# Optimization experiments

Measured on AMD Instinct MI355X. Metric: run time of the kernel, lower is better.

Reference implementation:

```python
import jax, jax.numpy as jnp
import numpy as np

D_IN, D_OUT, K = 128, 128, 64
X_MIN, X_MAX = 0.0, 1.0
EPS = 1e-12


def _pchip_slopes(y, x):
    # y: [..., K], x: [K] strictly increasing -> slopes [..., K]. Assumes K >= 3.
    h = x[1:] - x[:-1]                      # [K-1]
    delta = (y[..., 1:] - y[..., :-1]) / (h + EPS)
    h0, h1 = h[:-1], h[1:]
    w1 = 2.0 * h1 + h0
    w2 = h1 + 2.0 * h0
    d0_, d1_ = delta[..., :-1], delta[..., 1:]
    same_sign = d0_ * d1_ > 0
    denom = w1 / (d0_ + EPS) + w2 / (d1_ + EPS)
    d_int = jnp.where(same_sign, (w1 + w2) / (denom + EPS), 0.0)  # [..., K-2]
    d_first = ((2.0 * h[0] + h[1]) * delta[..., 0] - h[0] * delta[..., 1]) / (h[0] + h[1] + EPS)
    d_last = ((2.0 * h[-1] + h[-2]) * delta[..., -1] - h[-1] * delta[..., -2]) / (h[-1] + h[-2] + EPS)

    def limit(di, de):
        di = jnp.where(di * de <= 0, 0.0, di)
        return jnp.where(jnp.abs(di) > 3.0 * jnp.abs(de), 3.0 * de, di)

    d_first = limit(d_first, delta[..., 0])
    d_last = limit(d_last, delta[..., -1])
    return jnp.concatenate([d_first[..., None], d_int, d_last[..., None]], axis=-1)


def setup_inputs() -> dict:
    key = jax.random.key(0)
    k1, k2 = jax.random.split(key)
    x = jax.random.normal(k1, (4096, D_IN), dtype=jnp.float32)
    coeffs = 0.2 * jax.random.normal(k2, (D_OUT, D_IN, K), dtype=jnp.float32)
    bias = jnp.zeros((D_OUT,), dtype=jnp.float32)
    knots = jnp.linspace(X_MIN, X_MAX, K, dtype=jnp.float32)
    return {"x": x, "coeffs": coeffs, "bias": bias, "knots": knots}


def reference(x, coeffs, bias, knots):
    B = x.shape[0]
    slopes = _pchip_slopes(coeffs, knots)              # [d_out, d_in, K]
    h = (X_MAX - X_MIN) / (K - 1)

    xc = jnp.clip(x, X_MIN, X_MAX)                     # [B, d_in]
    idx = jnp.clip(jnp.floor((xc - X_MIN) / h).astype(jnp.int32), 0, K - 2)
    t = (xc - (X_MIN + idx.astype(x.dtype) * h)) / h   # [B, d_in]
    t2 = t * t
    t3 = t2 * t
    h00 = 2 * t3 - 3 * t2 + 1
    h10 = t3 - 2 * t2 + t
    h01 = -2 * t3 + 3 * t2
    h11 = t3 - t2

    ct = jnp.transpose(coeffs, (1, 2, 0))              # [d_in, K, d_out]
    dt = jnp.transpose(slopes, (1, 2, 0))              # [d_in, K, d_out]
    ii = jnp.arange(D_IN)[None, :]                     # [1, d_in]
    y0 = ct[ii, idx]                                   # [B, d_in, d_out]
    y1 = ct[ii, idx + 1]
    d0 = dt[ii, idx]
    d1 = dt[ii, idx + 1]

    yi = (h00[..., None] * y0 + h10[..., None] * h * d0
          + h01[..., None] * y1 + h11[..., None] * h * d1)  # [B, d_in, d_out]

    # linear extrapolation beyond the knot range
    y_left = ct[:, 0, :][None] + dt[:, 0, :][None] * (x - X_MIN)[..., None]
    y_right = ct[:, -1, :][None] + dt[:, -1, :][None] * (x - X_MAX)[..., None]
    yi = jnp.where((x < X_MIN)[..., None], y_left, yi)
    yi = jnp.where((x > X_MAX)[..., None], y_right, yi)

    return yi.sum(axis=1) + bias[None, :]              # [B, d_out]
```

## Files before the change

kernel.cpp:

```cpp
#include <hip/hip_runtime.h>
#include <hip/hip_fp16.h>

#define KN 64
#define DIN 128
#define DOUT 128
#define NJ 63
#define EPSF 1e-12f
#define HF (1.0f / 63.0f)


__global__ __launch_bounds__(256) void kan_precompute(
    const float* __restrict__ coeffs,
    const float* __restrict__ knots,
    uint2* __restrict__ pk)
{
    const int i      = blockIdx.x >> 1;
    const int o_base = (blockIdx.x & 1) << 6;
    const int wave   = threadIdx.x >> 6;
    const int lane   = threadIdx.x & 63;

    __shared__ float ys[64][65];
    __shared__ float ds[64][65];

    float kn  = knots[lane];
    float kn1 = (lane < 63) ? knots[lane + 1] : 0.0f;
    float hk  = kn1 - kn;
    float hm1 = __shfl_up(hk, 1);
    float h1v = __shfl_down(hk, 1);
    float hm2 = __shfl_up(hk, 2);

    for (int ol = wave; ol < 64; ol += 4) {
        const int o = o_base + ol;
        float y = coeffs[(o * DIN + i) * KN + lane];
        float ynext = __shfl_down(y, 1);
        float delta = (lane < 63) ? (ynext - y) / (hk + EPSF) : 0.0f;
        float dm1 = __shfl_up(delta, 1);

        float w1v = 2.0f * hk + hm1;
        float w2v = hk + 2.0f * hm1;
        float denom = w1v / (dm1 + EPSF) + w2v / (delta + EPSF);
        float d = (dm1 * delta > 0.0f) ? (w1v + w2v) / (denom + EPSF) : 0.0f;

        float d1v = __shfl_down(delta, 1);
        if (lane == 0) {
            float df = ((2.0f * hk + h1v) * delta - hk * d1v) / (hk + h1v + EPSF);
            if (df * delta <= 0.0f) df = 0.0f;
            else if (fabsf(df) > 3.0f * fabsf(delta)) df = 3.0f * delta;
            d = df;
        }
        float dm2 = __shfl_up(delta, 2);
        if (lane == 63) {
            float dl = ((2.0f * hm1 + hm2) * dm1 - hm1 * dm2) / (hm1 + hm2 + EPSF);
            if (dl * dm1 <= 0.0f) dl = 0.0f;
            else if (fabsf(dl) > 3.0f * fabsf(dm1)) dl = 3.0f * dm1;
            d = dl;
        }
        ys[ol][lane] = y;
        ds[ol][lane] = d * HF;
    }
    __syncthreads();

    const int ol = threadIdx.x & 63;
    const int jb = threadIdx.x >> 6;
    for (int j = jb; j < NJ; j += 4) {
        __half2 p0 = __floats2half2_rn(ys[ol][j],     ds[ol][j]);
        __half2 p1 = __floats2half2_rn(ys[ol][j + 1], ds[ol][j + 1]);
        uint2 v;
        v.x = *reinterpret_cast<unsigned int*>(&p0);
        v.y = *reinterpret_cast<unsigned int*>(&p1);
        pk[(i * NJ + j) * DOUT + o_base + ol] = v;
    }
}

__global__ __launch_bounds__(128) void kan_main(
    const float* __restrict__ x,
    const uint2* __restrict__ pk,
    const float* __restrict__ bias,
    float* __restrict__ out)
{
    const int b = blockIdx.x;
    const int o = threadIdx.x;

    __shared__ float4 wts[DIN];
    __shared__ int    idxs[DIN];

    const float h = HF;

    float xv = x[b * DIN + o];
    float xc = fminf(fmaxf(xv, 0.0f), 1.0f);
    int idx = (int)floorf(xc / h);
    idx = idx < 0 ? 0 : (idx > 62 ? 62 : idx);
    float t = (xc - (float)idx * h) / h;
    float t2 = t * t, t3 = t2 * t;
    float w0 = 2.0f * t3 - 3.0f * t2 + 1.0f;
    float w1 = t3 - 2.0f * t2 + t;
    float w2 = 3.0f * t2 - 2.0f * t3;
    float w3 = t3 - t2;
    if (xv < 0.0f)      { w0 = 1.0f; w1 = xv / h;          w2 = 0.0f; w3 = 0.0f;  idx = 0;  }
    else if (xv > 1.0f) { w0 = 0.0f; w1 = 0.0f; w2 = 1.0f; w3 = (xv - 1.0f) / h;  idx = 62; }
    wts[o]  = make_float4(w0, w1, w2, w3);
    idxs[o] = idx;
    __syncthreads();

    float acc0 = 0.0f, acc1 = 0.0f, acc2 = 0.0f, acc3 = 0.0f;
    #pragma unroll 4
    for (int i = 0; i < DIN; i += 4) {
        float4 wA = wts[i];     int jA = idxs[i];
        float4 wB = wts[i + 1]; int jB = idxs[i + 1];
        float4 wC = wts[i + 2]; int jC = idxs[i + 2];
        float4 wD = wts[i + 3]; int jD = idxs[i + 3];
        uint2 qA = pk[((i    ) * NJ + jA) * DOUT + o];
        uint2 qB = pk[((i + 1) * NJ + jB) * DOUT + o];
        uint2 qC = pk[((i + 2) * NJ + jC) * DOUT + o];
        uint2 qD = pk[((i + 3) * NJ + jD) * DOUT + o];
        float2 lA = __half22float2(*reinterpret_cast<const __half2*>(&qA.x));
        float2 hA = __half22float2(*reinterpret_cast<const __half2*>(&qA.y));
        float2 lB = __half22float2(*reinterpret_cast<const __half2*>(&qB.x));
        float2 hB = __half22float2(*reinterpret_cast<const __half2*>(&qB.y));
        float2 lC = __half22float2(*reinterpret_cast<const __half2*>(&qC.x));
        float2 hC = __half22float2(*reinterpret_cast<const __half2*>(&qC.y));
        float2 lD = __half22float2(*reinterpret_cast<const __half2*>(&qD.x));
        float2 hD = __half22float2(*reinterpret_cast<const __half2*>(&qD.y));
        acc0 += wA.x * lA.x + wA.y * lA.y + wA.z * hA.x + wA.w * hA.y;
        acc1 += wB.x * lB.x + wB.y * lB.y + wB.z * hB.x + wB.w * hB.y;
        acc2 += wC.x * lC.x + wC.y * lC.y + wC.z * hC.x + wC.w * hC.y;
        acc3 += wD.x * lD.x + wD.y * lD.y + wD.z * hD.x + wD.w * hD.y;
    }

    out[b * DOUT + o] = acc0 + acc1 + acc2 + acc3 + bias[o];
}

extern "C" void kernel_launch(void* const* d_in, const int* in_sizes, int n_in,
                              void* d_out, int out_size, void* d_ws, size_t ws_size,
                              hipStream_t stream) {
    const float* x      = (const float*)d_in[0];
    const float* coeffs = (const float*)d_in[1];
    const float* bias   = (const float*)d_in[2];
    const float* knots  = (const float*)d_in[3];
    float* out = (float*)d_out;
    uint2* pk = (uint2*)d_ws;

    kan_precompute<<<256, 256, 0, stream>>>(coeffs, knots, pk);
    kan_main<<<4096, 128, 0, stream>>>(x, pk, bias, out);
}
```

Baseline: 110.4 us.

## Repack spline table per knot, batch 4 rows per block, use fp16 dot2

The precomputed table now stores one (y, h*d) half2 per knot instead of duplicated per-interval pairs, which halves its size. In the main kernel each wave handles one batch row and each lane computes two outputs, loading two adjacent knots as uint2. The Hermite weights are kept in fp16 and accumulated with the fdot2 instruction. Four rows per 256-thread block cut the launch count. The cost is lower precision in the weights, since they are rounded to fp16 before the dot products.

Measured after the change: 107.5 us. 1.03x faster.

```diff
diff --git a/kernel.cpp b/kernel.cpp
--- a/kernel.cpp
+++ b/kernel.cpp
@@ -1,18 +1,29 @@
 #include <hip/hip_runtime.h>
-#include <hip/hip_fp16.h>
 
 #define KN 64
 #define DIN 128
 #define DOUT 128
-#define NJ 63
 #define EPSF 1e-12f
 #define HF (1.0f / 63.0f)
+
+typedef _Float16 h2 __attribute__((ext_vector_type(2)));
+
+#if defined(__has_builtin)
+#if __has_builtin(__builtin_amdgcn_fdot2)
+#define FDOT2(a, b, c) __builtin_amdgcn_fdot2((a), (b), (c), false)
+#endif
+#endif
+#ifndef FDOT2
+static __device__ __forceinline__ float FDOT2(h2 a, h2 b, float c) {
+    return c + (float)a.x * (float)b.x + (float)a.y * (float)b.y;
+}
+#endif
 
 
 __global__ __launch_bounds__(256) void kan_precompute(
     const float* __restrict__ coeffs,
     const float* __restrict__ knots,
-    uint2* __restrict__ pk)
+    unsigned int* __restrict__ tb)
 {
     const int i      = blockIdx.x >> 1;
     const int o_base = (blockIdx.x & 1) << 6;
@@ -61,73 +72,74 @@
     __syncthreads();
 
     const int ol = threadIdx.x & 63;
-    const int jb = threadIdx.x >> 6;
-    for (int j = jb; j < NJ; j += 4) {
-        __half2 p0 = __floats2half2_rn(ys[ol][j],     ds[ol][j]);
-        __half2 p1 = __floats2half2_rn(ys[ol][j + 1], ds[ol][j + 1]);
-        uint2 v;
-        v.x = *reinterpret_cast<unsigned int*>(&p0);
-        v.y = *reinterpret_cast<unsigned int*>(&p1);
-        pk[(i * NJ + j) * DOUT + o_base + ol] = v;
+    const int kb = threadIdx.x >> 6;
+    for (int k = kb; k < KN; k += 4) {
+        h2 v;
+        v.x = (_Float16)ys[ol][k];
+        v.y = (_Float16)ds[ol][k];
+        tb[(i * KN + k) * DOUT + o_base + ol] = __builtin_bit_cast(unsigned int, v);
     }
 }
 
-__global__ __launch_bounds__(128) void kan_main(
+__global__ __launch_bounds__(256) void kan_main(
     const float* __restrict__ x,
-    const uint2* __restrict__ pk,
+    const uint2* __restrict__ tb2,
     const float* __restrict__ bias,
     float* __restrict__ out)
 {
-    const int b = blockIdx.x;
-    const int o = threadIdx.x;
+    const int b0   = blockIdx.x << 2;
+    const int tid  = threadIdx.x;
+    const int wv   = tid >> 6;
+    const int lane = tid & 63;
 
-    __shared__ float4 wts[DIN];
-    __shared__ int    idxs[DIN];
+    __shared__ uint4 wl[4][DIN];
 
-    const float h = HF;
-
-    float xv = x[b * DIN + o];
-    float xc = fminf(fmaxf(xv, 0.0f), 1.0f);
-    int idx = (int)floorf(xc / h);
-    idx = idx < 0 ? 0 : (idx > 62 ? 62 : idx);
-    float t = (xc - (float)idx * h) / h;
-    float t2 = t * t, t3 = t2 * t;
-    float w0 = 2.0f * t3 - 3.0f * t2 + 1.0f;
-    float w1 = t3 - 2.0f * t2 + t;
-    float w2 = 3.0f * t2 - 2.0f * t3;
-    float w3 = t3 - t2;
-    if (xv < 0.0f)      { w0 = 1.0f; w1 = xv / h;          w2 = 0.0f; w3 = 0.0f;  idx = 0;  }
-    else if (xv > 1.0f) { w0 = 0.0f; w1 = 0.0f; w2 = 1.0f; w3 = (xv - 1.0f) / h;  idx = 62; }
-    wts[o]  = make_float4(w0, w1, w2, w3);
-    idxs[o] = idx;
+    #pragma unroll
+    for (int p = tid; p < 4 * DIN; p += 256) {
+        const int bl = p >> 7;
+        const int i  = p & 127;
+        float xv = x[(b0 + bl) * DIN + i];
+        float xc = fminf(fmaxf(xv, 0.0f), 1.0f);
+        int idx = (int)floorf(xc * 63.0f);
+        idx = idx < 0 ? 0 : (idx > 62 ? 62 : idx);
+        float t = xc * 63.0f - (float)idx;
+        float t2 = t * t, t3 = t2 * t;
+        float w0 = 2.0f * t3 - 3.0f * t2 + 1.0f;
+        float w1 = t3 - 2.0f * t2 + t;
+        float w2 = 3.0f * t2 - 2.0f * t3;
+        float w3 = t3 - t2;
+        if (xv < 0.0f)      { w0 = 1.0f; w1 = xv * 63.0f; w2 = 0.0f; w3 = 0.0f; idx = 0; }
+        else if (xv > 1.0f) { w0 = 0.0f; w1 = 0.0f; w2 = 1.0f; w3 = (xv - 1.0f) * 63.0f; idx = 62; }
+        h2 w01; w01.x = (_Float16)w0; w01.y = (_Float16)w1;
+        h2 w23; w23.x = (_Float16)w2; w23.y = (_Float16)w3;
+        uint4 q;
+        q.x = __builtin_bit_cast(unsigned int, w01);
+        q.y = __builtin_bit_cast(unsigned int, w23);
+        q.z = (unsigned int)idx;
+        q.w = 0u;
+        wl[bl][i] = q;
+    }
     __syncthreads();
 
-    float acc0 = 0.0f, acc1 = 0.0f, acc2 = 0.0f, acc3 = 0.0f;
-    #pragma unroll 4
-    for (int i = 0; i < DIN; i += 4) {
-        float4 wA = wts[i];     int jA = idxs[i];
-        float4 wB = wts[i + 1]; int jB = idxs[i + 1];
-        float4 wC = wts[i + 2]; int jC = idxs[i + 2];
-        float4 wD = wts[i + 3]; int jD = idxs[i + 3];
-        uint2 qA = pk[((i    ) * NJ + jA) * DOUT + o];
-        uint2 qB = pk[((i + 1) * NJ + jB) * DOUT + o];
-        uint2 qC = pk[((i + 2) * NJ + jC) * DOUT + o];
-        uint2 qD = pk[((i + 3) * NJ + jD) * DOUT + o];
-        float2 lA = __half22float2(*reinterpret_cast<const __half2*>(&qA.x));
-        float2 hA = __half22float2(*reinterpret_cast<const __half2*>(&qA.y));
-        float2 lB = __half22float2(*reinterpret_cast<const __half2*>(&qB.x));
-        float2 hB = __half22float2(*reinterpret_cast<const __half2*>(&qB.y));
-        float2 lC = __half22float2(*reinterpret_cast<const __half2*>(&qC.x));
-        float2 hC = __half22float2(*reinterpret_cast<const __half2*>(&qC.y));
-        float2 lD = __half22float2(*reinterpret_cast<const __half2*>(&qD.x));
-        float2 hD = __half22float2(*reinterpret_cast<const __half2*>(&qD.y));
-        acc0 += wA.x * lA.x + wA.y * lA.y + wA.z * hA.x + wA.w * hA.y;
-        acc1 += wB.x * lB.x + wB.y * lB.y + wB.z * hB.x + wB.w * hB.y;
-        acc2 += wC.x * lC.x + wC.y * lC.y + wC.z * hC.x + wC.w * hC.y;
-        acc3 += wD.x * lD.x + wD.y * lD.y + wD.z * hD.x + wD.w * hD.y;
+    float acc0 = 0.0f, acc1 = 0.0f;
+    #pragma unroll 8
+    for (int i = 0; i < DIN; ++i) {
+        uint4 q = wl[wv][i];
+        h2 w01 = __builtin_bit_cast(h2, q.x);
+        h2 w23 = __builtin_bit_cast(h2, q.y);
+        int base = ((i << 6) + (int)q.z) * 64 + lane;
+        uint2 A = tb2[base];
+        uint2 B = tb2[base + 64];
+        acc0 = FDOT2(w01, __builtin_bit_cast(h2, A.x), acc0);
+        acc0 = FDOT2(w23, __builtin_bit_cast(h2, B.x), acc0);
+        acc1 = FDOT2(w01, __builtin_bit_cast(h2, A.y), acc1);
+        acc1 = FDOT2(w23, __builtin_bit_cast(h2, B.y), acc1);
     }
 
-    out[b * DOUT + o] = acc0 + acc1 + acc2 + acc3 + bias[o];
+    const int o0 = lane << 1;
+    float2 bo = *reinterpret_cast<const float2*>(&bias[o0]);
+    float2 r; r.x = acc0 + bo.x; r.y = acc1 + bo.y;
+    *reinterpret_cast<float2*>(&out[(b0 + wv) * DOUT + o0]) = r;
 }
 
 extern "C" void kernel_launch(void* const* d_in, const int* in_sizes, int n_in,
@@ -138,8 +150,8 @@
     const float* bias   = (const float*)d_in[2];
     const float* knots  = (const float*)d_in[3];
     float* out = (float*)d_out;
-    uint2* pk = (uint2*)d_ws;
+    unsigned int* tb = (unsigned int*)d_ws;
 
-    kan_precompute<<<256, 256, 0, stream>>>(coeffs, knots, pk);
-    kan_main<<<4096, 128, 0, stream>>>(x, pk, bias, out);
+    kan_precompute<<<256, 256, 0, stream>>>(coeffs, knots, tb);
+    kan_main<<<1024, 256, 0, stream>>>(x, (const uint2*)tb, bias, out);
 }
```
